# Kernel optimization log

Measured on AMD Instinct MI355X. Metric: run time of the kernel, lower is better.

## Reference

```python
import jax, jax.numpy as jnp
import numpy as np

L2 = 65536          # edges per orientation (L=256 torus)
N = 2 * L2          # total edges
FIN = 8             # nfeatCNN_in
FOUT = 8            # nfeatCNN_out
K = 13              # kernel size (neighbor shifts per edge)
SCALE = (2.0 + 2.0 * np.e) / (np.e - 1.0)


def setup_inputs() -> dict:
    key = jax.random.key(0)
    ks = jax.random.split(key, 8)
    x = jax.random.normal(ks[0], (FIN * N,), dtype=jnp.float32)
    Wconv_hor = jax.random.normal(ks[1], (FOUT, FIN, K), dtype=jnp.float32) * 0.1
    Wconv_vert = jax.random.normal(ks[2], (FOUT, FIN, K), dtype=jnp.float32) * 0.1
    bconv_hor = jnp.zeros((FOUT,), dtype=jnp.float32)
    bconv_vert = jnp.zeros((FOUT,), dtype=jnp.float32)
    mask_hor = jax.random.randint(ks[3], (L2, FOUT, FIN, K), 0, 2).astype(bool)
    mask_vert = jax.random.randint(ks[4], (L2, FOUT, FIN, K), 0, 2).astype(bool)
    ker_hor = jax.random.randint(ks[5], (L2, K), 0, N, dtype=jnp.int32)
    ker_vert = jax.random.randint(ks[6], (L2, K), 0, N, dtype=jnp.int32)
    hor_edge_lst = jnp.arange(L2, dtype=jnp.int32)
    vert_edge_lst = jnp.arange(L2, dtype=jnp.int32) + L2
    return {
        "x": x,
        "Wconv_hor": Wconv_hor, "Wconv_vert": Wconv_vert,
        "bconv_hor": bconv_hor, "bconv_vert": bconv_vert,
        "mask_hor": mask_hor, "mask_vert": mask_vert,
        "ker_hor": ker_hor, "ker_vert": ker_vert,
        "hor_edge_lst": hor_edge_lst, "vert_edge_lst": vert_edge_lst,
    }


def reference(x, Wconv_hor, Wconv_vert, bconv_hor, bconv_vert,
              mask_hor, mask_vert, ker_hor, ker_vert,
              hor_edge_lst, vert_edge_lst):
    fout, fin, _ = Wconv_hor.shape
    n = x.shape[0] // fin
    xm = x.reshape(fin, n)                      # (fin, N)

    def branch(W, mask, ker, b):
        xg = xm[:, ker]                         # gather -> (fin, E, K)
        Wm = W[None] * mask.astype(W.dtype)     # (E, fout, fin, K)
        # per-edge masked contraction over (fin, K); vectorized over edges
        z = jnp.einsum('eoik,iek->oe', Wm, xg)  # (fout, E)
        return z + b[:, None]

    x_hor = branch(Wconv_hor, mask_hor, ker_hor, bconv_hor)
    x_vert = branch(Wconv_vert, mask_vert, ker_vert, bconv_vert)

    out = jnp.zeros((fout, n), dtype=x.dtype)
    out = out.at[:, hor_edge_lst].set(x_hor)
    out = out.at[:, vert_edge_lst].set(x_vert)
    return (jax.nn.sigmoid(out) - 0.5) * jnp.asarray(SCALE, out.dtype)
```

## Files before the change

kernel.cpp:

```cpp
#include <hip/hip_runtime.h>
#include <math.h>

#define L2C   65536
#define NC    (2 * L2C)
#define FINC  8
#define FOUTC 8
#define KC    13
#define BLOCK 256
#define EPB   4

constexpr double E_D = 2.71828182845904523536;
constexpr float SCALE_F = (float)((2.0 + 2.0 * E_D) / (E_D - 1.0));


__global__ __launch_bounds__(256)
void transpose_x_kernel(const float* __restrict__ x, float* __restrict__ xt) {
    int n = blockIdx.x * 256 + threadIdx.x;
    float v[FINC];
#pragma unroll
    for (int i = 0; i < FINC; ++i) v[i] = x[(size_t)i * NC + n];
    float4* dst = reinterpret_cast<float4*>(xt + ((size_t)n << 3));
    dst[0] = make_float4(v[0], v[1], v[2], v[3]);
    dst[1] = make_float4(v[4], v[5], v[6], v[7]);
}

__global__ __launch_bounds__(BLOCK)
void edge_conv_kernel(const float* __restrict__ xt,
                      const float* __restrict__ Wh, const float* __restrict__ Wv,
                      const float* __restrict__ bh, const float* __restrict__ bv,
                      const unsigned char* __restrict__ mh,
                      const unsigned char* __restrict__ mv,
                      const int* __restrict__ kh, const int* __restrict__ kv,
                      float* __restrict__ out)
{
    __shared__ float Wsh[FOUTC * FINC * KC];

    const int tid  = threadIdx.x;
    const int lane = tid & 63;
    const int o    = lane >> 3;
    const int i    = lane & 7;

    const int blk = blockIdx.x;
    const int blocks_per_branch = L2C / EPB;
    const bool hor = (blk < blocks_per_branch);

    const float*         W    = hor ? Wh  : Wv;
    const float*         bias = hor ? bh  : bv;
    const unsigned char* mask = hor ? mh  : mv;
    const int*           ker  = hor ? kh  : kv;
    const int bblk = hor ? blk : blk - blocks_per_branch;
    const int be   = bblk * EPB + (tid >> 6);
    const int col  = hor ? be : (be + L2C);

    for (int j = tid; j < FOUTC * FINC * KC; j += BLOCK) Wsh[j] = W[j];

    const unsigned char probe = mh[(size_t)(lane * 4 + 1)];
    const bool words = (__ballot(probe != 0) == 0ull);

    __syncthreads();

    unsigned long long myb = 0;
    if (words) {
        const unsigned int* mw = reinterpret_cast<const unsigned int*>(mask)
                                 + (size_t)be * 832;
        const uint4* mw4 = reinterpret_cast<const uint4*>(mw);
        const uint4 s0 = mw4[lane];
        const uint4 s1 = mw4[64 + lane];
        const uint4 s2 = mw4[128 + lane];
        const unsigned int t3 = mw[768 + lane];

        const int packed =
              (int)(s0.x != 0u)        | ((int)(s0.y != 0u) << 1)
            | ((int)(s0.z != 0u) << 2) | ((int)(s0.w != 0u) << 3)
            | ((int)(s1.x != 0u) << 4) | ((int)(s1.y != 0u) << 5)
            | ((int)(s1.z != 0u) << 6) | ((int)(s1.w != 0u) << 7)
            | ((int)(s2.x != 0u) << 8) | ((int)(s2.y != 0u) << 9)
            | ((int)(s2.z != 0u) << 10)| ((int)(s2.w != 0u) << 11);

#pragma unroll
        for (int u = 0; u < 12; ++u) {
            const int src = ((u & 3) << 4) + (lane >> 2);
            const int pk  = __shfl(packed, src);
            const int bit = (pk >> (((u >> 2) << 2) + (lane & 3))) & 1;
            const unsigned long long bal = __ballot(bit != 0);
            if (lane == u) myb = bal;
        }
        {
            const unsigned long long bal = __ballot(t3 != 0u);
            if (lane == 12) myb = bal;
        }
    } else {
        const unsigned char* mb = mask + (size_t)be * 832 + lane;
#pragma unroll
        for (int t = 0; t < KC; ++t) {
            unsigned long long bal = __ballot(mb[t * 64] != 0);
            if (lane == t) myb = bal;
        }
    }

    int cols[KC];
#pragma unroll
    for (int k = 0; k < KC; ++k) cols[k] = ker[(size_t)be * KC + k];

    const int s     = lane * KC;
    const int u0    = s >> 6;
    const int shift = s & 63;
    unsigned long long lo = __shfl(myb, u0);
    unsigned long long hi = __shfl(myb, u0 + 1);
    unsigned int mbits = (unsigned int)(lo >> shift);
    if (shift) mbits |= (unsigned int)(hi << (64 - shift));
    mbits &= 0x1FFFu;

    float acc = 0.0f;
#pragma unroll
    for (int k = 0; k < KC; ++k) {
        const float xv = xt[((size_t)cols[k] << 3) + i];
        const float wk = Wsh[lane * KC + k];
        const float wm = ((mbits >> k) & 1u) ? wk : 0.0f;
        acc = fmaf(wm, xv, acc);
    }

    acc += __shfl_xor(acc, 1);
    acc += __shfl_xor(acc, 2);
    acc += __shfl_xor(acc, 4);

    if (i == 0) {
        const float z   = acc + bias[o];
        const float sig = 1.0f / (1.0f + __expf(-z));
        out[(size_t)o * NC + col] = (sig - 0.5f) * SCALE_F;
    }
}

extern "C" void kernel_launch(void* const* d_in, const int* in_sizes, int n_in,
                              void* d_out, int out_size, void* d_ws, size_t ws_size,
                              hipStream_t stream) {
    const float*         x   = (const float*)d_in[0];
    const float*         Wh  = (const float*)d_in[1];
    const float*         Wv  = (const float*)d_in[2];
    const float*         bh  = (const float*)d_in[3];
    const float*         bv  = (const float*)d_in[4];
    const unsigned char* mh  = (const unsigned char*)d_in[5];
    const unsigned char* mv  = (const unsigned char*)d_in[6];
    const int*           kh  = (const int*)d_in[7];
    const int*           kv  = (const int*)d_in[8];
    float* out = (float*)d_out;
    float* xt  = (float*)d_ws;

    transpose_x_kernel<<<NC / 256, 256, 0, stream>>>(x, xt);
    edge_conv_kernel<<<NC / EPB, BLOCK, 0, stream>>>(
        xt, Wh, Wv, bh, bv, mh, mv, kh, kv, out);
}
```

Before: 451.3 us.

## Pre-pack boolean masks into a bitmap in a separate kernel before convolution

Adds a pack kernel that compresses both boolean mask tensors into a compact bitmap in the workspace, and a conv kernel that reads 13 mask bits per lane from that bitmap instead of ballot-packing raw mask bytes. The aim is to strip mask decoding and its wide loads out of the gather/FMA kernel. The cost is an extra kernel launch plus a bitmap write and read, and the new path only runs if the workspace is large enough. The fallback kernel's word path is also simplified to per-word ballots.

```diff
diff --git a/kernel.cpp b/kernel.cpp
--- a/kernel.cpp
+++ b/kernel.cpp
@@ -12,6 +12,11 @@
 constexpr double E_D = 2.71828182845904523536;
 constexpr float SCALE_F = (float)((2.0 + 2.0 * E_D) / (E_D - 1.0));
 
+#define WORDS_PER_BRANCH        ((size_t)L2C * FOUTC * FINC * KC)
+#define PACK_THREADS_PER_BRANCH (WORDS_PER_BRANCH / 4)
+#define BITMAP_BYTES_PER_BRANCH (WORDS_PER_BRANCH / 8)
+#define XT_BYTES                ((size_t)NC * FINC * 4)
+
 
 __global__ __launch_bounds__(256)
 void transpose_x_kernel(const float* __restrict__ x, float* __restrict__ xt) {
@@ -22,6 +27,101 @@
     float4* dst = reinterpret_cast<float4*>(xt + ((size_t)n << 3));
     dst[0] = make_float4(v[0], v[1], v[2], v[3]);
     dst[1] = make_float4(v[4], v[5], v[6], v[7]);
+}
+
+__global__ __launch_bounds__(256)
+void pack_mask_kernel(const unsigned char* __restrict__ mh,
+                      const unsigned char* __restrict__ mv,
+                      unsigned char* __restrict__ bm)
+{
+    const int lane = threadIdx.x & 63;
+    const unsigned char probe = mh[(size_t)(lane * 4 + 1)];
+    const bool words = (__ballot(probe != 0) == 0ull);
+
+    const size_t t   = (size_t)blockIdx.x * 256 + threadIdx.x;
+    const bool   hor = t < PACK_THREADS_PER_BRANCH;
+    const unsigned char* src = hor ? mh : mv;
+    const size_t u   = hor ? t : t - PACK_THREADS_PER_BRANCH;
+    unsigned char* dst = bm + (hor ? 0 : BITMAP_BYTES_PER_BRANCH);
+
+    unsigned int nib;
+    if (words) {
+        const uint4 v = reinterpret_cast<const uint4*>(src)[u];
+        nib =  (unsigned int)(v.x != 0u)
+            | ((unsigned int)(v.y != 0u) << 1)
+            | ((unsigned int)(v.z != 0u) << 2)
+            | ((unsigned int)(v.w != 0u) << 3);
+    } else {
+        const unsigned int v = reinterpret_cast<const unsigned int*>(src)[u];
+        nib =  (unsigned int)((v & 0x000000FFu) != 0u)
+            | ((unsigned int)((v & 0x0000FF00u) != 0u) << 1)
+            | ((unsigned int)((v & 0x00FF0000u) != 0u) << 2)
+            | ((unsigned int)((v & 0xFF000000u) != 0u) << 3);
+    }
+    nib |= ((unsigned int)__shfl_down((int)nib, 1)) << 4;
+    if ((u & 1) == 0) dst[u >> 1] = (unsigned char)nib;
+}
+
+__global__ __launch_bounds__(BLOCK)
+void edge_conv_bitmap_kernel(const float* __restrict__ xt,
+                             const float* __restrict__ Wh, const float* __restrict__ Wv,
+                             const float* __restrict__ bh, const float* __restrict__ bv,
+                             const unsigned char* __restrict__ bm,
+                             const int* __restrict__ kh, const int* __restrict__ kv,
+                             float* __restrict__ out)
+{
+    __shared__ float Wsh[FOUTC * FINC * KC];
+
+    const int tid  = threadIdx.x;
+    const int lane = tid & 63;
+    const int o    = lane >> 3;
+    const int i    = lane & 7;
+
+    const int blk = blockIdx.x;
+    const int blocks_per_branch = L2C / EPB;
+    const bool hor = (blk < blocks_per_branch);
+
+    const float* W    = hor ? Wh : Wv;
+    const float* bias = hor ? bh : bv;
+    const int*   ker  = hor ? kh : kv;
+    const int bblk = hor ? blk : blk - blocks_per_branch;
+    const int be   = bblk * EPB + (tid >> 6);
+    const int col  = hor ? be : (be + L2C);
+
+    for (int j = tid; j < FOUTC * FINC * KC; j += BLOCK) Wsh[j] = W[j];
+
+    const unsigned int* bmw = reinterpret_cast<const unsigned int*>(bm)
+                              + (hor ? 0 : (BITMAP_BYTES_PER_BRANCH / 4));
+    const int g = be * (FOUTC * FINC * KC) + lane * KC;
+    const unsigned int blo = bmw[g >> 5];
+    const unsigned int bhi = bmw[(g >> 5) + 1];
+    const unsigned int mbits =
+        (unsigned int)((((unsigned long long)bhi << 32) | blo) >> (g & 31)) & 0x1FFFu;
+
+    int cols[KC];
+#pragma unroll
+    for (int k = 0; k < KC; ++k) cols[k] = ker[(size_t)be * KC + k];
+
+    __syncthreads();
+
+    float acc = 0.0f;
+#pragma unroll
+    for (int k = 0; k < KC; ++k) {
+        const float xv = xt[((size_t)cols[k] << 3) + i];
+        const float wk = Wsh[lane * KC + k];
+        const float wm = ((mbits >> k) & 1u) ? wk : 0.0f;
+        acc = fmaf(wm, xv, acc);
+    }
+
+    acc += __shfl_xor(acc, 1);
+    acc += __shfl_xor(acc, 2);
+    acc += __shfl_xor(acc, 4);
+
+    if (i == 0) {
+        const float z   = acc + bias[o];
+        const float sig = 1.0f / (1.0f + __expf(-z));
+        out[(size_t)o * NC + col] = (sig - 0.5f) * SCALE_F;
+    }
 }
 
 __global__ __launch_bounds__(BLOCK)
@@ -62,32 +162,11 @@
     unsigned long long myb = 0;
     if (words) {
         const unsigned int* mw = reinterpret_cast<const unsigned int*>(mask)
-                                 + (size_t)be * 832;
-        const uint4* mw4 = reinterpret_cast<const uint4*>(mw);
-        const uint4 s0 = mw4[lane];
-        const uint4 s1 = mw4[64 + lane];
-        const uint4 s2 = mw4[128 + lane];
-        const unsigned int t3 = mw[768 + lane];
-
-        const int packed =
-              (int)(s0.x != 0u)        | ((int)(s0.y != 0u) << 1)
-            | ((int)(s0.z != 0u) << 2) | ((int)(s0.w != 0u) << 3)
-            | ((int)(s1.x != 0u) << 4) | ((int)(s1.y != 0u) << 5)
-            | ((int)(s1.z != 0u) << 6) | ((int)(s1.w != 0u) << 7)
-            | ((int)(s2.x != 0u) << 8) | ((int)(s2.y != 0u) << 9)
-            | ((int)(s2.z != 0u) << 10)| ((int)(s2.w != 0u) << 11);
-
-#pragma unroll
-        for (int u = 0; u < 12; ++u) {
-            const int src = ((u & 3) << 4) + (lane >> 2);
-            const int pk  = __shfl(packed, src);
-            const int bit = (pk >> (((u >> 2) << 2) + (lane & 3))) & 1;
-            const unsigned long long bal = __ballot(bit != 0);
-            if (lane == u) myb = bal;
-        }
-        {
-            const unsigned long long bal = __ballot(t3 != 0u);
-            if (lane == 12) myb = bal;
+                                 + (size_t)be * 832 + lane;
+#pragma unroll
+        for (int t = 0; t < KC; ++t) {
+            unsigned long long bal = __ballot(mw[t * 64] != 0u);
+            if (lane == t) myb = bal;
         }
     } else {
         const unsigned char* mb = mask + (size_t)be * 832 + lane;
@@ -147,6 +226,16 @@
     float* xt  = (float*)d_ws;
 
     transpose_x_kernel<<<NC / 256, 256, 0, stream>>>(x, xt);
-    edge_conv_kernel<<<NC / EPB, BLOCK, 0, stream>>>(
-        xt, Wh, Wv, bh, bv, mh, mv, kh, kv, out);
-}
+
+    const size_t needed = XT_BYTES + 2 * BITMAP_BYTES_PER_BRANCH + 64;
+    if (ws_size >= needed) {
+        unsigned char* bm = (unsigned char*)d_ws + XT_BYTES;
+        pack_mask_kernel<<<(unsigned)((2 * PACK_THREADS_PER_BRANCH) / 256), 256, 0, stream>>>(
+            mh, mv, bm);
+        edge_conv_bitmap_kernel<<<NC / EPB, BLOCK, 0, stream>>>(
+            xt, Wh, Wv, bh, bv, bm, kh, kv, out);
+    } else {
+        edge_conv_kernel<<<NC / EPB, BLOCK, 0, stream>>>(
+            xt, Wh, Wv, bh, bv, mh, mv, kh, kv, out);
+    }
+}
```

New measurement: 499.7 us. 10.7% more time.

## Stage per-block mask tile in LDS instead of ballot-based bit packing

Applied to the files above, without the earlier changes.

Replaces the shuffle/ballot mask bit-packing with a cooperative block-wide uint4 copy of the four edges' contiguous mask words into shared memory. Each lane then reads its 13 mask entries directly from LDS. The weight load is vectorized to float4, and the FMA chain is split into two accumulators to shorten the dependency chain. This removes the many cross-lane ops and per-wave strided loads, at the cost of about 13 KB of LDS per block, which may reduce occupancy, plus possible LDS bank conflicts from the stride-13 row reads.

```diff
diff --git a/kernel.cpp b/kernel.cpp
--- a/kernel.cpp
+++ b/kernel.cpp
@@ -8,6 +8,7 @@
 #define KC    13
 #define BLOCK 256
 #define EPB   4
+#define EWORDS (FOUTC * FINC * KC)
 
 constexpr double E_D = 2.71828182845904523536;
 constexpr float SCALE_F = (float)((2.0 + 2.0 * E_D) / (E_D - 1.0));
@@ -33,10 +34,12 @@
                       const int* __restrict__ kh, const int* __restrict__ kv,
                       float* __restrict__ out)
 {
-    __shared__ float Wsh[FOUTC * FINC * KC];
+    __shared__ float        Wsh[EWORDS];
+    __shared__ unsigned int msh[EPB * EWORDS];
 
     const int tid  = threadIdx.x;
     const int lane = tid & 63;
+    const int wave = tid >> 6;
     const int o    = lane >> 3;
     const int i    = lane & 7;
 
@@ -49,76 +52,60 @@
     const unsigned char* mask = hor ? mh  : mv;
     const int*           ker  = hor ? kh  : kv;
     const int bblk = hor ? blk : blk - blocks_per_branch;
-    const int be   = bblk * EPB + (tid >> 6);
+    const int be   = bblk * EPB + wave;
     const int col  = hor ? be : (be + L2C);
-
-    for (int j = tid; j < FOUTC * FINC * KC; j += BLOCK) Wsh[j] = W[j];
-
-    const unsigned char probe = mh[(size_t)(lane * 4 + 1)];
-    const bool words = (__ballot(probe != 0) == 0ull);
-
-    __syncthreads();
-
-    unsigned long long myb = 0;
-    if (words) {
-        const unsigned int* mw = reinterpret_cast<const unsigned int*>(mask)
-                                 + (size_t)be * 832;
-        const uint4* mw4 = reinterpret_cast<const uint4*>(mw);
-        const uint4 s0 = mw4[lane];
-        const uint4 s1 = mw4[64 + lane];
-        const uint4 s2 = mw4[128 + lane];
-        const unsigned int t3 = mw[768 + lane];
-
-        const int packed =
-              (int)(s0.x != 0u)        | ((int)(s0.y != 0u) << 1)
-            | ((int)(s0.z != 0u) << 2) | ((int)(s0.w != 0u) << 3)
-            | ((int)(s1.x != 0u) << 4) | ((int)(s1.y != 0u) << 5)
-            | ((int)(s1.z != 0u) << 6) | ((int)(s1.w != 0u) << 7)
-            | ((int)(s2.x != 0u) << 8) | ((int)(s2.y != 0u) << 9)
-            | ((int)(s2.z != 0u) << 10)| ((int)(s2.w != 0u) << 11);
-
-#pragma unroll
-        for (int u = 0; u < 12; ++u) {
-            const int src = ((u & 3) << 4) + (lane >> 2);
-            const int pk  = __shfl(packed, src);
-            const int bit = (pk >> (((u >> 2) << 2) + (lane & 3))) & 1;
-            const unsigned long long bal = __ballot(bit != 0);
-            if (lane == u) myb = bal;
-        }
-        {
-            const unsigned long long bal = __ballot(t3 != 0u);
-            if (lane == 12) myb = bal;
-        }
-    } else {
-        const unsigned char* mb = mask + (size_t)be * 832 + lane;
-#pragma unroll
-        for (int t = 0; t < KC; ++t) {
-            unsigned long long bal = __ballot(mb[t * 64] != 0);
-            if (lane == t) myb = bal;
-        }
-    }
 
     int cols[KC];
 #pragma unroll
     for (int k = 0; k < KC; ++k) cols[k] = ker[(size_t)be * KC + k];
 
-    const int s     = lane * KC;
-    const int u0    = s >> 6;
-    const int shift = s & 63;
-    unsigned long long lo = __shfl(myb, u0);
-    unsigned long long hi = __shfl(myb, u0 + 1);
-    unsigned int mbits = (unsigned int)(lo >> shift);
-    if (shift) mbits |= (unsigned int)(hi << (64 - shift));
-    mbits &= 0x1FFFu;
+    const unsigned char probe = mh[(size_t)(lane * 4 + 1)];
+    const bool words = (__ballot(probe != 0) == 0ull);
 
-    float acc = 0.0f;
+    if (words) {
+        const uint4* g4 = reinterpret_cast<const uint4*>(
+            mask + (size_t)bblk * (EPB * EWORDS * 4));
+        uint4* m4 = reinterpret_cast<uint4*>(msh);
 #pragma unroll
-    for (int k = 0; k < KC; ++k) {
-        const float xv = xt[((size_t)cols[k] << 3) + i];
-        const float wk = Wsh[lane * KC + k];
-        const float wm = ((mbits >> k) & 1u) ? wk : 0.0f;
-        acc = fmaf(wm, xv, acc);
+        for (int idx = tid; idx < EPB * EWORDS / 4; idx += BLOCK)
+            m4[idx] = g4[idx];
+    } else {
+        const uint4* g4 = reinterpret_cast<const uint4*>(
+            mask + (size_t)bblk * (EPB * EWORDS));
+        uint4* m4 = reinterpret_cast<uint4*>(msh);
+        if (tid < EPB * EWORDS / 16)
+            m4[tid] = g4[tid];
     }
+
+    if (tid < EWORDS / 4)
+        reinterpret_cast<float4*>(Wsh)[tid] = reinterpret_cast<const float4*>(W)[tid];
+
+    __syncthreads();
+
+    float acc0 = 0.0f, acc1 = 0.0f;
+    if (words) {
+        const unsigned int* mrow = msh + wave * EWORDS + lane * KC;
+#pragma unroll
+        for (int k = 0; k < KC; ++k) {
+            const float xv = xt[((size_t)cols[k] << 3) + i];
+            const float wk = Wsh[lane * KC + k];
+            const float wm = mrow[k] ? wk : 0.0f;
+            if (k & 1) acc1 = fmaf(wm, xv, acc1);
+            else       acc0 = fmaf(wm, xv, acc0);
+        }
+    } else {
+        const unsigned char* mrow = reinterpret_cast<const unsigned char*>(msh)
+                                    + wave * EWORDS + lane * KC;
+#pragma unroll
+        for (int k = 0; k < KC; ++k) {
+            const float xv = xt[((size_t)cols[k] << 3) + i];
+            const float wk = Wsh[lane * KC + k];
+            const float wm = mrow[k] ? wk : 0.0f;
+            if (k & 1) acc1 = fmaf(wm, xv, acc1);
+            else       acc0 = fmaf(wm, xv, acc0);
+        }
+    }
+    float acc = acc0 + acc1;
 
     acc += __shfl_xor(acc, 1);
     acc += __shfl_xor(acc, 2);
```

After: 458.7 us. No clear change (+1.7%).
